# Kernel optimization log

Measured on AMD Instinct MI355X. Metric: run time of the kernel, lower is better.

The kernel has to match this reference:

```python
import jax, jax.numpy as jnp
import numpy as np
from jax.scipy.special import erf

F = 64          # scalar feature channels (hidden_irreps multiplicity)
S = 9           # spherical harmonics dim for max_ell=2
NB = 8          # num_bessel
RMAX = 5.0
PPOLY = 5       # num_polynomial_cutoff
AVG_NEIGH = 16.0
SIGMA = 1.0     # atomic_multipoles_smearing_width
KE = 1.0        # Coulomb constant (model units)
N = 20000; G = 20; E = 320000; NEL = 10; L = 2; HMLP = 16

def _sph_l2(u):
    # real spherical harmonics up to l=2, e3nn 'component' normalization,
    # with permute_to_e3nn_convention (y, z, x) ordering for l=1
    x, y, z = u[..., 0], u[..., 1], u[..., 2]
    s3 = 1.7320508075688772; s5 = 2.23606797749979; s15 = 3.872983346207417
    return jnp.stack([jnp.ones_like(x),
                      s3 * y, s3 * z, s3 * x,
                      s15 * x * y, s15 * y * z, 0.5 * s5 * (3.0 * z * z - 1.0),
                      s15 * x * z, 0.5 * s15 * (x * x - y * y)], axis=-1)

def _radial(r):
    # Bessel basis with smooth polynomial cutoff (p = PPOLY)
    n = jnp.arange(1, NB + 1, dtype=r.dtype)
    rb = jnp.sqrt(2.0 / RMAX) * jnp.sin(n * jnp.pi * r[:, None] / RMAX) / r[:, None]
    x = r / RMAX
    p = float(PPOLY)
    u = (1.0 - 0.5 * (p + 1.0) * (p + 2.0) * x**PPOLY
         + p * (p + 2.0) * x**(PPOLY + 1) - 0.5 * p * (p + 1.0) * x**(PPOLY + 2))
    u = jnp.where(x < 1.0, u, 0.0)
    return rb * u[:, None]

def setup_inputs() -> dict:
    key = jax.random.key(0)
    ks = jax.random.split(key, 20)
    Ng = N // G
    species = jax.random.randint(ks[0], (N,), 0, NEL)
    node_attrs = jax.nn.one_hot(species, NEL, dtype=jnp.float32)
    positions = jax.random.uniform(ks[1], (N, 3), dtype=jnp.float32) * 10.0
    g = jax.random.randint(ks[2], (E,), 0, G)
    s_loc = jax.random.randint(ks[3], (E,), 0, Ng)
    off = jax.random.randint(ks[4], (E,), 1, Ng)   # avoid self edges
    r_loc = (s_loc + off) % Ng
    edge_index = jnp.stack([g * Ng + s_loc, g * Ng + r_loc], axis=0)
    batch = jnp.repeat(jnp.arange(G), Ng)
    sc = 0.1
    atomic_energies = jax.random.normal(ks[5], (NEL,)) * sc
    embed_w = jax.random.normal(ks[6], (NEL, F)) * sc
    radial_w1 = jax.random.normal(ks[7], (L, NB, 64)) * 0.3
    radial_b1 = jnp.zeros((L, 64), jnp.float32)
    radial_w2 = jax.random.normal(ks[8], (L, 64, F)) * 0.2
    prod_w = jax.random.normal(ks[9], (L, NEL, F)) * 0.3
    readout_w = jax.random.normal(ks[10], (L, F)) * sc
    ro2_w1 = jax.random.normal(ks[11], (F, HMLP)) * 0.2
    ro2_b1 = jnp.zeros((HMLP,), jnp.float32)
    ro2_w2 = jax.random.normal(ks[12], (HMLP, 1)) * 0.2
    charge_w = jax.random.normal(ks[13], (L, F)) * sc
    flux_w = jax.random.normal(ks[14], (L, NB)) * sc
    formal_charges = jax.random.normal(ks[15], (NEL,)) * 0.5
    return dict(node_attrs=node_attrs, positions=positions, edge_index=edge_index,
                batch=batch, num_graphs=G, atomic_energies=atomic_energies,
                embed_w=embed_w, radial_w1=radial_w1, radial_b1=radial_b1,
                radial_w2=radial_w2, prod_w=prod_w, readout_w=readout_w,
                ro2_w1=ro2_w1, ro2_b1=ro2_b1, ro2_w2=ro2_w2,
                charge_w=charge_w, flux_w=flux_w, formal_charges=formal_charges)

def reference(node_attrs, positions, edge_index, batch, num_graphs,
              atomic_energies, embed_w, radial_w1, radial_b1, radial_w2,
              prod_w, readout_w, ro2_w1, ro2_b1, ro2_w2,
              charge_w, flux_w, formal_charges):
    Nn = node_attrs.shape[0]
    Ng = Nn // num_graphs
    snd, rcv = edge_index[0], edge_index[1]
    # atomic reference energies (E0) and node embedding
    node_e0 = node_attrs @ atomic_energies                      # [N]
    e0 = jax.ops.segment_sum(node_e0, batch, num_graphs)        # [G]
    node_scalars = node_attrs @ embed_w                         # [N,F]
    # edge geometry: gather, spherical harmonics, radial embedding
    vec = positions[rcv] - positions[snd]                       # [E,3]
    lengths = jnp.sqrt((vec * vec).sum(-1) + 1e-12)             # [E]
    unit = vec / lengths[:, None]
    edge_attrs = _sph_l2(unit)                                  # [E,S]
    edge_feats = _radial(lengths)                               # [E,NB]
    # formal charges (per-species)
    FQ = node_attrs @ formal_charges                            # [N]
    charge_density = FQ
    flux = jnp.zeros_like(lengths)
    energies = [e0]
    node_e_list = [node_e0]
    nL = radial_w1.shape[0]
    for l in range(nL):
        # interaction: radial MLP -> per-edge TP messages -> scatter sum
        R = jax.nn.silu(edge_feats @ radial_w1[l] + radial_b1[l]) @ radial_w2[l]  # [E,F]
        m = (R * node_scalars[snd])[:, :, None] * edge_attrs[:, None, :]          # [E,F,S]
        agg = jax.ops.segment_sum(m, rcv, Nn) / AVG_NEIGH                         # [N,F,S]
        # equivariant product (correlation-2 flavor) + element-dependent skip
        sk = node_scalars * (node_attrs @ prod_w[l])                              # [N,F]
        feats = agg + agg * agg[:, :, :1]                                         # [N,F,S]
        node_scalars = feats[:, :, 0] + sk                                        # [N,F]
        if l == nL - 1:
            node_energies = (jax.nn.silu(node_scalars @ ro2_w1 + ro2_b1) @ ro2_w2)[:, 0]
        else:
            node_energies = node_scalars @ readout_w[l]
        energies.append(jax.ops.segment_sum(node_energies, batch, num_graphs))
        node_e_list.append(node_energies)
        # long-range source maps: per-node charge + per-edge flux contributions
        charge_density = charge_density + node_scalars @ charge_w[l]
        flux = flux + edge_feats @ flux_w[l]
    contributions = jnp.stack(energies, -1)                     # [G, L+1]
    total_energy = contributions.sum(-1)                        # [G]
    node_energy = jnp.stack(node_e_list, -1).sum(-1)            # [N]
    # polarization: edge-flux dipole + formal-charge dipole
    pol = jax.ops.segment_sum(flux[:, None] * vec, batch[rcv], num_graphs)
    pol = pol + jax.ops.segment_sum(FQ[:, None] * positions, batch, num_graphs)
    # direct (non-PBC) screened Coulomb energy per graph, equal-size graphs
    q = charge_density.reshape(num_graphs, Ng)
    p = positions.reshape(num_graphs, Ng, 3)
    d = p[:, :, None, :] - p[:, None, :, :]
    r = jnp.sqrt((d * d).sum(-1) + 1e-12)
    kern = erf(r / (2.0 * SIGMA)) / r * (1.0 - jnp.eye(Ng, dtype=r.dtype))
    e_el = 0.5 * KE * jnp.einsum('gi,gij,gj->g', q, kern, q)
    total_energy = total_energy + e_el
    total_charge = jax.ops.segment_sum(charge_density, batch, num_graphs)
    return total_energy, node_energy, contributions, pol, total_charge
```

## Files before the change

kernel.cpp:

```cpp
#include <hip/hip_runtime.h>
#include <math.h>

#define NEL 10
#define FD 64
#define NBES 8
#define GG 20
#define HML 16
#define EGB 512
#define NUB 5000

typedef __attribute__((ext_vector_type(8))) short short8;
typedef __attribute__((ext_vector_type(4))) float f32x4;

__device__ __forceinline__ float wred(float v) {
    #pragma unroll
    for (int off = 32; off > 0; off >>= 1) v += __shfl_down(v, off, 64);
    return v;
}

__device__ __forceinline__ float silu(float h) {
    return h / (1.f + __expf(-h));
}

__device__ __forceinline__ unsigned short f2bf(float x) {
    unsigned int b = __float_as_uint(x);
    unsigned int r = (b + 0x7FFFu + ((b >> 16) & 1u)) >> 16;
    return (unsigned short)r;
}

__global__ __launch_bounds__(256) void setup_k(
    const float* __restrict__ attrs, const float* __restrict__ ae,
    const float* __restrict__ fc, const float* __restrict__ embed_w,
    const int* __restrict__ eidx, int* __restrict__ spec,
    float* __restrict__ q, float* __restrict__ out,
    float* __restrict__ scal, float* __restrict__ agg0,
    int* __restrict__ cnt, int N_, int E_)
{
    int idx = blockIdx.x * 256 + threadIdx.x;
    int lane = threadIdx.x & 63;
    int n = idx >> 6;
    bool pred = (lane < NEL) && (attrs[(size_t)n * NEL + lane] > 0.5f);
    unsigned long long m = __ballot(pred);
    int sp = (int)__builtin_ctzll(m);
    scal[idx] = embed_w[sp * FD + lane];
    agg0[idx] = 0.f;
    if (lane == 0) { spec[n] = sp; q[n] = fc[sp]; out[GG + n] = ae[sp]; }
    if (idx < E_) atomicAdd(&cnt[eidx[E_ + idx]], 1);
    if (idx < GG) out[idx] = 0.f;
}

__global__ __launch_bounds__(1024) void scan_k(
    const int* __restrict__ cnt, int* __restrict__ cur,
    const float* __restrict__ w1, const float* __restrict__ w2,
    unsigned short* __restrict__ w1bf, unsigned short* __restrict__ w2bf, int N_)
{
    int t = threadIdx.x;
    #pragma unroll
    for (int ii = 0; ii < 8; ++ii) {
        int idx = ii * 1024 + t;
        int l = idx >> 12, rem = idx & 4095;
        int f = rem >> 6, k = rem & 63;
        w2bf[idx] = f2bf(w2[l * 4096 + k * 64 + f]);
    }
    {
        int l = t >> 9, rem = t & 511;
        int m = rem >> 3, j = rem & 7;
        w1bf[t] = f2bf(w1[l * 512 + j * 64 + m]);
    }
    __shared__ int wtot[16];
    int lane = t & 63, wid = t >> 6;
    int base = t * 20;
    int c[20]; int s = 0;
    #pragma unroll
    for (int i = 0; i < 20; ++i) { int idx = base + i; c[i] = (idx < N_) ? cnt[idx] : 0; s += c[i]; }
    int v = s;
    #pragma unroll
    for (int off = 1; off < 64; off <<= 1) {
        int u = __shfl_up(v, off, 64);
        if (lane >= off) v += u;
    }
    if (lane == 63) wtot[wid] = v;
    __syncthreads();
    if (wid == 0 && lane < 16) {
        int wv = wtot[lane];
        #pragma unroll
        for (int off = 1; off < 16; off <<= 1) {
            int u = __shfl_up(wv, off, 64);
            if (lane >= off) wv += u;
        }
        wtot[lane] = wv;
    }
    __syncthreads();
    int ex = (wid > 0 ? wtot[wid - 1] : 0) + (v - s);
    #pragma unroll
    for (int i = 0; i < 20; ++i) {
        int idx = base + i;
        if (idx < N_) { cur[idx] = ex; ex += c[i]; }
    }
}

__global__ __launch_bounds__(256) void geom_scatter_k(
    const float* __restrict__ pos, const int* __restrict__ eidx,
    const float* __restrict__ flux_w, int* __restrict__ cur,
    int* __restrict__ snd_s, int* __restrict__ rcv_s,
    unsigned short* __restrict__ ef_bf, float* __restrict__ polpart,
    int E_, int ng)
{
    __shared__ float lpol[GG * 3];
    int tid = threadIdx.x;
    for (int i = tid; i < GG * 3; i += 256) lpol[i] = 0.f;
    __syncthreads();
    float fw[NBES];
    #pragma unroll
    for (int i = 0; i < NBES; ++i) fw[i] = flux_w[i] + flux_w[NBES + i];
    const float PI = 3.14159265358979323846f;
    for (int e = blockIdx.x * 256 + tid; e < E_; e += EGB * 256) {
        int s = eidx[e], r = eidx[E_ + e];
        float dx = pos[(size_t)r*3+0] - pos[(size_t)s*3+0];
        float dy = pos[(size_t)r*3+1] - pos[(size_t)s*3+1];
        float dz = pos[(size_t)r*3+2] - pos[(size_t)s*3+2];
        float len = sqrtf(dx*dx + dy*dy + dz*dz + 1e-12f);
        float x = len * 0.2f;
        float u = 0.f;
        if (x < 1.f) {
            float x2 = x * x;
            float x5 = x2 * x2 * x;
            u = 1.f - 21.f * x5 + 35.f * x5 * x - 15.f * x5 * x2;
        }
        float pref = 0.6324555320336759f / len * u;
        float theta = PI * x;
        float s1, c1;
        __sincosf(theta, &s1, &c1);
        float c2 = 2.f * c1;
        float sp_ = 0.f, sn = s1;
        float flux = 0.f;
        unsigned int pk[4];
        #pragma unroll
        for (int i = 0; i < 4; ++i) {
            float r0 = pref * sn;
            float n1 = c2 * sn - sp_; sp_ = sn; sn = n1;
            float r1 = pref * sn;
            n1 = c2 * sn - sp_; sp_ = sn; sn = n1;
            flux += r0 * fw[2*i] + r1 * fw[2*i+1];
            pk[i] = (unsigned int)f2bf(r0) | ((unsigned int)f2bf(r1) << 16);
        }
        int p = atomicAdd(&cur[r], 1);
        *(uint4*)&ef_bf[(size_t)p * NBES] = make_uint4(pk[0], pk[1], pk[2], pk[3]);
        snd_s[p] = s;
        rcv_s[p] = r;
        int g = r / ng;
        atomicAdd(&lpol[g*3+0], flux * dx);
        atomicAdd(&lpol[g*3+1], flux * dy);
        atomicAdd(&lpol[g*3+2], flux * dz);
    }
    __syncthreads();
    for (int i = tid; i < GG * 3; i += 256) polpart[blockIdx.x * (GG * 3) + i] = lpol[i];
}

__global__ __launch_bounds__(256, 8) void edge_mlp_k(
    const unsigned short* __restrict__ ef_bf, const int* __restrict__ snd_s,
    const int* __restrict__ rcv_s,
    const unsigned short* __restrict__ w1bf, const float* __restrict__ b1,
    const unsigned short* __restrict__ w2bf, const float* __restrict__ scal,
    float* __restrict__ agg0, int layer, int E_)
{
    __shared__ __align__(16) char smem[4][4352];
    int t = threadIdx.x, w = t >> 6, lane = t & 63;
    int mrow = lane & 15, quad = lane >> 4;
    int ebase = (blockIdx.x * 4 + w) * 16;
    unsigned short* hw = (unsigned short*)smem[w];
    float* cw = (float*)smem[w];

    int sv = snd_s[ebase + mrow];
    int rv = rcv_s[ebase + mrow];

    const short8 z8 = {0,0,0,0,0,0,0,0};
    short8 b_ef = z8;
    if (quad == 0) b_ef = *(const short8*)&ef_bf[(size_t)(ebase + mrow) * NBES];
    else if (quad == 1) b_ef[0] = (short)0x3F80;
    short8 a1f[4];
    #pragma unroll
    for (int nt = 0; nt < 4; ++nt) {
        a1f[nt] = z8;
        if (quad == 0) a1f[nt] = *(const short8*)&w1bf[layer * 512 + (nt * 16 + mrow) * 8];
        else if (quad == 1) a1f[nt][0] = (short)f2bf(b1[layer * FD + nt * 16 + mrow]);
    }
    const unsigned short* wb = w2bf + layer * 4096;
    short8 bf0[4], bf1[4];
    #pragma unroll
    for (int nt = 0; nt < 4; ++nt) {
        bf0[nt] = *(const short8*)&wb[(nt * 16 + mrow) * 64 + quad * 8];
        bf1[nt] = *(const short8*)&wb[(nt * 16 + mrow) * 64 + 32 + quad * 8];
    }

    f32x4 zf = {0.f, 0.f, 0.f, 0.f};
    #pragma unroll
    for (int nt = 0; nt < 4; ++nt) {
        f32x4 c1 = __builtin_amdgcn_mfma_f32_16x16x32_bf16(a1f[nt], b_ef, zf, 0, 0, 0);
        unsigned int p01 = (unsigned int)f2bf(silu(c1[0])) | ((unsigned int)f2bf(silu(c1[1])) << 16);
        unsigned int p23 = (unsigned int)f2bf(silu(c1[2])) | ((unsigned int)f2bf(silu(c1[3])) << 16);
        *(uint2*)&hw[mrow * 72 + nt * 16 + quad * 4] = make_uint2(p01, p23);
    }

    short8 a0  = *(const short8*)&hw[mrow * 72 + quad * 8];
    short8 a1b = *(const short8*)&hw[mrow * 72 + 32 + quad * 8];
    f32x4 c[4];
    #pragma unroll
    for (int nt = 0; nt < 4; ++nt) {
        f32x4 cc = __builtin_amdgcn_mfma_f32_16x16x32_bf16(a0, bf0[nt], zf, 0, 0, 0);
        cc = __builtin_amdgcn_mfma_f32_16x16x32_bf16(a1b, bf1[nt], cc, 0, 0, 0);
        c[nt] = cc;
    }
    #pragma unroll
    for (int nt = 0; nt < 4; ++nt)
        #pragma unroll
        for (int reg = 0; reg < 4; ++reg)
            cw[(quad * 4 + reg) * 68 + nt * 16 + mrow] = c[nt][reg];

    int curR = __builtin_amdgcn_readlane(rv, 0);
    float run = 0.f;
    #pragma unroll
    for (int half = 0; half < 2; ++half) {
        float cv[8], sw[8];
        #pragma unroll
        for (int k = 0; k < 8; ++k) {
            int pp = half * 8 + k;
            cv[k] = cw[pp * 68 + lane];
            int s = __builtin_amdgcn_readlane(sv, pp);
            sw[k] = scal[(size_t)s * FD + lane];
        }
        #pragma unroll
        for (int k = 0; k < 8; ++k) {
            int pp = half * 8 + k;
            int r = __builtin_amdgcn_readlane(rv, pp);
            float v = cv[k] * sw[k];
            if (r != curR) {
                atomicAdd(&agg0[(size_t)curR * FD + lane], run);
                run = v; curR = r;
            } else {
                run += v;
            }
        }
    }
    atomicAdd(&agg0[(size_t)curR * FD + lane], run);
}

__global__ __launch_bounds__(256) void node_update_k(
    float* __restrict__ scal, float* __restrict__ agg0,
    const int* __restrict__ spec, const float* __restrict__ prod_w,
    const float* __restrict__ readout_w, const float* __restrict__ ro2_w1,
    const float* __restrict__ ro2_b1, const float* __restrict__ ro2_w2,
    const float* __restrict__ charge_w, float* __restrict__ q,
    float* __restrict__ out_nodeE, float* __restrict__ nEpart,
    int layer, int last, int N_)
{
    __shared__ float vsh[4][FD];
    __shared__ float red[4];
    int wid = threadIdx.x >> 6, lane = threadIdx.x & 63;
    int n = blockIdx.x * 4 + wid;
    int sp = spec[n];
    size_t idx = (size_t)n * FD + lane;
    float a = agg0[idx] * 0.0625f;
    agg0[idx] = 0.f;
    float v = a + a * a + scal[idx] * prod_w[(layer * NEL + sp) * FD + lane];
    scal[idx] = v;

    float ne;
    if (!last) {
        ne = wred(v * readout_w[layer * FD + lane]);
    } else {
        vsh[wid][lane] = v;
        float h = 0.f;
        if (lane < HML) {
            h = ro2_b1[lane];
            for (int ff = 0; ff < FD; ++ff) h += vsh[wid][ff] * ro2_w1[ff * HML + lane];
            h = silu(h) * ro2_w2[lane];
        }
        ne = wred(h);
    }
    float qs = wred(v * charge_w[layer * FD + lane]);
    if (lane == 0) {
        out_nodeE[n] += ne;
        q[n] += qs;
        red[wid] = ne;
    }
    __syncthreads();
    if (threadIdx.x == 0) nEpart[layer * NUB + blockIdx.x] = red[0] + red[1] + red[2] + red[3];
}

__global__ __launch_bounds__(256) void coulomb_final_k(
    const float* __restrict__ q, const float* __restrict__ pos,
    const int* __restrict__ spec, const float* __restrict__ ae,
    const float* __restrict__ fc, const float* __restrict__ nEpart,
    const float* __restrict__ polpart, float* __restrict__ out,
    int N_, int ng)
{
    __shared__ float sh[260];
    int vb = blockIdx.x;
    int g = vb / 137, rem = vb % 137;
    int t = threadIdx.x, lane = t & 63, w = t >> 6;

    if (rem < 136) {
        int a = 0, r2 = rem;
        while (r2 >= 16 - a) { r2 -= 16 - a; ++a; }
        int b = a + r2;
        const float* qg = q + (size_t)g * ng;
        const float* pg = pos + (size_t)g * ng * 3;
        float* qs_ = sh; float* jx = sh + 64; float* jy = sh + 128; float* jz = sh + 192;
        if (t < 64) {
            int j = b * 64 + t;
            bool ok = j < ng;
            qs_[t] = ok ? qg[j] : 0.f;
            jx[t] = ok ? pg[(size_t)j*3+0] : 0.f;
            jy[t] = ok ? pg[(size_t)j*3+1] : 0.f;
            jz[t] = ok ? pg[(size_t)j*3+2] : 0.f;
        }
        __syncthreads();
        int i = a * 64 + lane;
        float accu = 0.f;
        if (i < ng) {
            float qi = qg[i];
            float xi = pg[(size_t)i*3+0], yi = pg[(size_t)i*3+1], zi = pg[(size_t)i*3+2];
            #pragma unroll 4
            for (int k = 0; k < 16; ++k) {
                int jj = w * 16 + k;
                int j = b * 64 + jj;
                float dx = xi - jx[jj], dy = yi - jy[jj], dz = zi - jz[jj];
                float d2 = dx*dx + dy*dy + dz*dz + 1e-12f;
                float rinv = __frsqrt_rn(d2);
                float r = d2 * rinv;
                float x = 0.5f * r;
                float tt = __frcp_rn(1.f + 0.3275911f * x);
                float poly = ((((1.061405429f*tt - 1.453152027f)*tt + 1.421413741f)*tt
                               - 0.284496736f)*tt + 0.254829592f)*tt;
                float erfv = 1.f - poly * __expf(-x * x);
                float kern = (j == i) ? 0.f : erfv * rinv;
                accu += qi * qs_[jj] * kern;
            }
        }
        accu = wred(accu);
        if (lane == 0) sh[256 + w] = accu;
        __syncthreads();
        if (t == 0) {
            float s = sh[256] + sh[257] + sh[258] + sh[259];
            atomicAdd(&out[g], (a == b) ? 0.5f * s : s);
        }
    } else {
        float se0 = 0.f, sq = 0.f, p0 = 0.f, p1 = 0.f, p2 = 0.f, s0 = 0.f, s1 = 0.f;
        for (int n = g * ng + t; n < (g + 1) * ng; n += 256) {
            int sp = spec[n];
            float fq = fc[sp];
            se0 += ae[sp];
            sq += q[n];
            p0 += fq * pos[(size_t)n*3+0];
            p1 += fq * pos[(size_t)n*3+1];
            p2 += fq * pos[(size_t)n*3+2];
        }
        if (t < 250) {
            int b = g * 250 + t;
            s0 = nEpart[b];
            s1 = nEpart[NUB + b];
        }
        for (int b = t; b < EGB; b += 256) {
            p0 += polpart[b * (GG * 3) + g * 3 + 0];
            p1 += polpart[b * (GG * 3) + g * 3 + 1];
            p2 += polpart[b * (GG * 3) + g * 3 + 2];
        }
        float vals[7] = {se0, s0, s1, sq, p0, p1, p2};
        float* red = sh;
        #pragma unroll
        for (int k = 0; k < 7; ++k) {
            float r = wred(vals[k]);
            if (lane == 0) red[w * 8 + k] = r;
        }
        __syncthreads();
        if (t < 7) sh[64 + t] = red[t] + red[8 + t] + red[16 + t] + red[24 + t];
        __syncthreads();
        if (t == 0) {
            float a0 = sh[64], a1 = sh[65], a2 = sh[66];
            atomicAdd(&out[g], a0 + a1 + a2);
            float* contrib = out + GG + N_;
            contrib[g*3+0] = a0; contrib[g*3+1] = a1; contrib[g*3+2] = a2;
            float* pol = contrib + GG * 3;
            pol[g*3+0] = sh[68]; pol[g*3+1] = sh[69]; pol[g*3+2] = sh[70];
            float* qt = pol + GG * 3;
            qt[g] = sh[67];
        }
    }
}

extern "C" void kernel_launch(void* const* d_in, const int* in_sizes, int n_in,
                              void* d_out, int out_size, void* d_ws, size_t ws_size,
                              hipStream_t stream)
{
    const float* node_attrs      = (const float*)d_in[0];
    const float* positions       = (const float*)d_in[1];
    const int*   edge_index      = (const int*)d_in[2];
    const float* atomic_energies = (const float*)d_in[5];
    const float* embed_w         = (const float*)d_in[6];
    const float* radial_w1       = (const float*)d_in[7];
    const float* radial_b1       = (const float*)d_in[8];
    const float* radial_w2       = (const float*)d_in[9];
    const float* prod_w          = (const float*)d_in[10];
    const float* readout_w       = (const float*)d_in[11];
    const float* ro2_w1          = (const float*)d_in[12];
    const float* ro2_b1          = (const float*)d_in[13];
    const float* ro2_w2          = (const float*)d_in[14];
    const float* charge_w        = (const float*)d_in[15];
    const float* flux_w          = (const float*)d_in[16];
    const float* formal_charges  = (const float*)d_in[17];

    int N = in_sizes[0] / NEL;
    int E = in_sizes[2] / 2;
    int ng = N / GG;

    float* ws      = (float*)d_ws;
    float* scal    = ws;
    float* agg0    = scal + (size_t)N * FD;
    unsigned short* ef_bf = (unsigned short*)(agg0 + (size_t)N * FD);
    float* q       = (float*)(ef_bf + (size_t)E * NBES);
    int*   spec    = (int*)(q + N);
    float* nEpart  = (float*)(spec + N);
    float* polpart = nEpart + 2 * NUB;
    int*   cnt     = (int*)(polpart + EGB * (GG * 3));
    int*   cur     = cnt + N;
    int*   snd_s   = cur + N;
    int*   rcv_s   = snd_s + E;
    unsigned short* w2bf = (unsigned short*)(rcv_s + E);
    unsigned short* w1bf = w2bf + 8192;

    float* out = (float*)d_out;
    float* out_nodeE = out + GG;

    hipMemsetAsync(cnt, 0, (size_t)N * sizeof(int), stream);

    setup_k<<<(N * FD) / 256, 256, 0, stream>>>(
        node_attrs, atomic_energies, formal_charges, embed_w, edge_index,
        spec, q, out, scal, agg0, cnt, N, E);
    scan_k<<<1, 1024, 0, stream>>>(cnt, cur, radial_w1, radial_w2, w1bf, w2bf, N);
    geom_scatter_k<<<EGB, 256, 0, stream>>>(
        positions, edge_index, flux_w, cur, snd_s, rcv_s, ef_bf, polpart, E, ng);

    for (int l = 0; l < 2; ++l) {
        edge_mlp_k<<<E / 64, 256, 0, stream>>>(
            ef_bf, snd_s, rcv_s, w1bf, radial_b1, w2bf, scal, agg0, l, E);
        node_update_k<<<N / 4, 256, 0, stream>>>(
            scal, agg0, spec, prod_w, readout_w, ro2_w1, ro2_b1, ro2_w2,
            charge_w, q, out_nodeE, nEpart, l, (l == 1) ? 1 : 0, N);
    }

    coulomb_final_k<<<GG * 137, 256, 0, stream>>>(
        q, positions, spec, atomic_energies, formal_charges,
        nEpart, polpart, out, N, ng);
}
```

Measured before the change: 284.4 us.

## Pack edge features and indices into one record, swizzle blocks across XCDs

```diff
diff --git a/kernel.cpp b/kernel.cpp
--- a/kernel.cpp
+++ b/kernel.cpp
@@ -26,6 +26,12 @@
     unsigned int b = __float_as_uint(x);
     unsigned int r = (b + 0x7FFFu + ((b >> 16) & 1u)) >> 16;
     return (unsigned short)r;
+}
+
+__device__ __forceinline__ int xcd_swizzle(int bid, int nb) {
+    int q = nb >> 3, r = nb & 7;
+    int x = bid & 7, i = bid >> 3;
+    return (x < r ? x * (q + 1) : r * (q + 1) + (x - r) * q) + i;
 }
 
 __global__ __launch_bounds__(256) void setup_k(
@@ -71,8 +77,19 @@
     int lane = t & 63, wid = t >> 6;
     int base = t * 20;
     int c[20]; int s = 0;
-    #pragma unroll
-    for (int i = 0; i < 20; ++i) { int idx = base + i; c[i] = (idx < N_) ? cnt[idx] : 0; s += c[i]; }
+    bool full = (base + 20 <= N_);
+    if (full) {
+        #pragma unroll
+        for (int i = 0; i < 5; ++i) {
+            int4 v4 = *(const int4*)&cnt[base + i * 4];
+            c[i*4+0] = v4.x; c[i*4+1] = v4.y; c[i*4+2] = v4.z; c[i*4+3] = v4.w;
+        }
+        #pragma unroll
+        for (int i = 0; i < 20; ++i) s += c[i];
+    } else {
+        #pragma unroll
+        for (int i = 0; i < 20; ++i) { int idx = base + i; c[i] = (idx < N_) ? cnt[idx] : 0; s += c[i]; }
+    }
     int v = s;
     #pragma unroll
     for (int off = 1; off < 64; off <<= 1) {
@@ -92,18 +109,26 @@
     }
     __syncthreads();
     int ex = (wid > 0 ? wtot[wid - 1] : 0) + (v - s);
-    #pragma unroll
-    for (int i = 0; i < 20; ++i) {
-        int idx = base + i;
-        if (idx < N_) { cur[idx] = ex; ex += c[i]; }
+    if (full) {
+        int o[20];
+        #pragma unroll
+        for (int i = 0; i < 20; ++i) { o[i] = ex; ex += c[i]; }
+        #pragma unroll
+        for (int i = 0; i < 5; ++i)
+            *(int4*)&cur[base + i * 4] = make_int4(o[i*4+0], o[i*4+1], o[i*4+2], o[i*4+3]);
+    } else {
+        #pragma unroll
+        for (int i = 0; i < 20; ++i) {
+            int idx = base + i;
+            if (idx < N_) { cur[idx] = ex; ex += c[i]; }
+        }
     }
 }
 
 __global__ __launch_bounds__(256) void geom_scatter_k(
     const float* __restrict__ pos, const int* __restrict__ eidx,
     const float* __restrict__ flux_w, int* __restrict__ cur,
-    int* __restrict__ snd_s, int* __restrict__ rcv_s,
-    unsigned short* __restrict__ ef_bf, float* __restrict__ polpart,
+    unsigned int* __restrict__ esd, float* __restrict__ polpart,
     int E_, int ng)
 {
     __shared__ float lpol[GG * 3];
@@ -145,9 +170,9 @@
             pk[i] = (unsigned int)f2bf(r0) | ((unsigned int)f2bf(r1) << 16);
         }
         int p = atomicAdd(&cur[r], 1);
-        *(uint4*)&ef_bf[(size_t)p * NBES] = make_uint4(pk[0], pk[1], pk[2], pk[3]);
-        snd_s[p] = s;
-        rcv_s[p] = r;
+        size_t off = (size_t)p * 8;
+        *(uint4*)&esd[off]     = make_uint4(pk[0], pk[1], pk[2], pk[3]);
+        *(uint2*)&esd[off + 4] = make_uint2((unsigned int)s, (unsigned int)r);
         int g = r / ng;
         atomicAdd(&lpol[g*3+0], flux * dx);
         atomicAdd(&lpol[g*3+1], flux * dy);
@@ -157,9 +182,8 @@
     for (int i = tid; i < GG * 3; i += 256) polpart[blockIdx.x * (GG * 3) + i] = lpol[i];
 }
 
-__global__ __launch_bounds__(256, 8) void edge_mlp_k(
-    const unsigned short* __restrict__ ef_bf, const int* __restrict__ snd_s,
-    const int* __restrict__ rcv_s,
+__global__ __launch_bounds__(256, 6) void edge_mlp_k(
+    const unsigned int* __restrict__ esd,
     const unsigned short* __restrict__ w1bf, const float* __restrict__ b1,
     const unsigned short* __restrict__ w2bf, const float* __restrict__ scal,
     float* __restrict__ agg0, int layer, int E_)
@@ -167,16 +191,17 @@
     __shared__ __align__(16) char smem[4][4352];
     int t = threadIdx.x, w = t >> 6, lane = t & 63;
     int mrow = lane & 15, quad = lane >> 4;
-    int ebase = (blockIdx.x * 4 + w) * 16;
+    int xb = xcd_swizzle(blockIdx.x, gridDim.x);
+    int ebase = (xb * 4 + w) * 16;
     unsigned short* hw = (unsigned short*)smem[w];
     float* cw = (float*)smem[w];
 
-    int sv = snd_s[ebase + mrow];
-    int rv = rcv_s[ebase + mrow];
+    int2 sr = *(const int2*)&esd[(size_t)(ebase + mrow) * 8 + 4];
+    int sv = sr.x, rv = sr.y;
 
     const short8 z8 = {0,0,0,0,0,0,0,0};
     short8 b_ef = z8;
-    if (quad == 0) b_ef = *(const short8*)&ef_bf[(size_t)(ebase + mrow) * NBES];
+    if (quad == 0) b_ef = *(const short8*)&esd[(size_t)(ebase + mrow) * 8];
     else if (quad == 1) b_ef[0] = (short)0x3F80;
     short8 a1f[4];
     #pragma unroll
@@ -184,13 +209,6 @@
         a1f[nt] = z8;
         if (quad == 0) a1f[nt] = *(const short8*)&w1bf[layer * 512 + (nt * 16 + mrow) * 8];
         else if (quad == 1) a1f[nt][0] = (short)f2bf(b1[layer * FD + nt * 16 + mrow]);
-    }
-    const unsigned short* wb = w2bf + layer * 4096;
-    short8 bf0[4], bf1[4];
-    #pragma unroll
-    for (int nt = 0; nt < 4; ++nt) {
-        bf0[nt] = *(const short8*)&wb[(nt * 16 + mrow) * 64 + quad * 8];
-        bf1[nt] = *(const short8*)&wb[(nt * 16 + mrow) * 64 + 32 + quad * 8];
     }
 
     f32x4 zf = {0.f, 0.f, 0.f, 0.f};
@@ -200,6 +218,14 @@
         unsigned int p01 = (unsigned int)f2bf(silu(c1[0])) | ((unsigned int)f2bf(silu(c1[1])) << 16);
         unsigned int p23 = (unsigned int)f2bf(silu(c1[2])) | ((unsigned int)f2bf(silu(c1[3])) << 16);
         *(uint2*)&hw[mrow * 72 + nt * 16 + quad * 4] = make_uint2(p01, p23);
+    }
+
+    const unsigned short* wb = w2bf + layer * 4096;
+    short8 bf0[4], bf1[4];
+    #pragma unroll
+    for (int nt = 0; nt < 4; ++nt) {
+        bf0[nt] = *(const short8*)&wb[(nt * 16 + mrow) * 64 + quad * 8];
+        bf1[nt] = *(const short8*)&wb[(nt * 16 + mrow) * 64 + 32 + quad * 8];
     }
 
     short8 a0  = *(const short8*)&hw[mrow * 72 + quad * 8];
@@ -261,7 +287,7 @@
     int sp = spec[n];
     size_t idx = (size_t)n * FD + lane;
     float a = agg0[idx] * 0.0625f;
-    agg0[idx] = 0.f;
+    if (!last) agg0[idx] = 0.f;
     float v = a + a * a + scal[idx] * prod_w[(layer * NEL + sp) * FD + lane];
     scal[idx] = v;
 
@@ -417,16 +443,14 @@
     float* ws      = (float*)d_ws;
     float* scal    = ws;
     float* agg0    = scal + (size_t)N * FD;
-    unsigned short* ef_bf = (unsigned short*)(agg0 + (size_t)N * FD);
-    float* q       = (float*)(ef_bf + (size_t)E * NBES);
+    unsigned int* esd = (unsigned int*)(agg0 + (size_t)N * FD);
+    float* q       = (float*)(esd + (size_t)E * 8);
     int*   spec    = (int*)(q + N);
     float* nEpart  = (float*)(spec + N);
     float* polpart = nEpart + 2 * NUB;
     int*   cnt     = (int*)(polpart + EGB * (GG * 3));
     int*   cur     = cnt + N;
-    int*   snd_s   = cur + N;
-    int*   rcv_s   = snd_s + E;
-    unsigned short* w2bf = (unsigned short*)(rcv_s + E);
+    unsigned short* w2bf = (unsigned short*)(cur + N);
     unsigned short* w1bf = w2bf + 8192;
 
     float* out = (float*)d_out;
@@ -439,11 +463,11 @@
         spec, q, out, scal, agg0, cnt, N, E);
     scan_k<<<1, 1024, 0, stream>>>(cnt, cur, radial_w1, radial_w2, w1bf, w2bf, N);
     geom_scatter_k<<<EGB, 256, 0, stream>>>(
-        positions, edge_index, flux_w, cur, snd_s, rcv_s, ef_bf, polpart, E, ng);
+        positions, edge_index, flux_w, cur, esd, polpart, E, ng);
 
     for (int l = 0; l < 2; ++l) {
         edge_mlp_k<<<E / 64, 256, 0, stream>>>(
-            ef_bf, snd_s, rcv_s, w1bf, radial_b1, w2bf, scal, agg0, l, E);
+            esd, w1bf, radial_b1, w2bf, scal, agg0, l, E);
         node_update_k<<<N / 4, 256, 0, stream>>>(
             scal, agg0, spec, prod_w, readout_w, ro2_w1, ro2_b1, ro2_w2,
             charge_w, q, out_nodeE, nEpart, l, (l == 1) ? 1 : 0, N);
```

After: 271.3 us. 1.05x faster.
